# Performance work log

Measured on AMD Instinct MI355X. Metric: run time of the kernel, lower is better.

Reference implementation:

```python
import jax, jax.numpy as jnp
import numpy as np

NUM_Q = 8
K = 1024          # codebook_size
D = 256           # latent_dim
N = 65536         # number of vectors
COMMIT = 0.25


def setup_inputs() -> dict:
    key = jax.random.key(0)
    kz, kc = jax.random.split(key)
    z = jax.random.normal(kz, (N, D), dtype=jnp.float32)
    # torch init: uniform(-1/K, 1/K) per quantizer
    codebooks = jax.random.uniform(kc, (NUM_Q, K, D), dtype=jnp.float32,
                                   minval=-1.0 / K, maxval=1.0 / K)
    return {"z": z, "codebooks": codebooks}


def _vq_step(residual, W):
    # residual: [N, D], W: [K, D]
    # squared L2 distances [N, K] (same expansion as the torch code)
    d = (jnp.sum(residual ** 2, axis=1, keepdims=True)
         + jnp.sum(W ** 2, axis=1)
         - 2.0 * residual @ W.T)
    idx = jnp.argmin(d, axis=1)                      # [N]
    zq = W[idx]                                      # gather == one-hot @ W
    zq_ste = residual + jax.lax.stop_gradient(zq - residual)
    commitment = jnp.mean((jax.lax.stop_gradient(residual) - zq) ** 2)
    codebook_l = jnp.mean((residual - jax.lax.stop_gradient(zq)) ** 2)
    loss = codebook_l + COMMIT * commitment
    return zq_ste, idx, loss


def reference(z, codebooks):
    def step(residual, W):
        zq_ste, idx, loss = _vq_step(residual, W)
        residual_new = residual - jax.lax.stop_gradient(zq_ste)
        return residual_new, (zq_ste, idx, loss)

    _, (all_q, all_idx, losses) = jax.lax.scan(step, z, codebooks)
    z_reconstructed = jnp.sum(all_q, axis=0)          # [N, D]
    final_indices = all_idx.T[:, :, None]             # [N, Q, 1] (torch stacks [N,1] on dim=1)
    total_loss = jnp.sum(losses)
    return z_reconstructed, final_indices, total_loss
```

## Files before the change

### kernel.cpp

```cpp
#include <hip/hip_runtime.h>
#include <stdint.h>


#define NQ      8
#define KCODES  1024
#define DIM     256
#define NVEC    65536
#define ROWS    32
#define RST     260
#define CCH     32
#define CAP     32

typedef unsigned int u32;
typedef unsigned long long u64;
typedef unsigned short u16;
typedef short bf16x8 __attribute__((ext_vector_type(8)));
typedef float f32x4  __attribute__((ext_vector_type(4)));

__device__ float  g_norms[NQ * KCODES];
__device__ u32    g_nkmax;
__device__ double g_loss;
__device__ __align__(16) u16 g_wb[(size_t)NQ * KCODES * DIM];

__device__ __forceinline__ u16 bf16rne(float x){
    u32 u = __float_as_uint(x);
    return (u16)((u + 0x7FFFu + ((u >> 16) & 1u)) >> 16);
}

__device__ __forceinline__ void gload_lds16(const void* g, void* l){
    __builtin_amdgcn_global_load_lds(
        (const __attribute__((address_space(1))) u32*)g,
        (__attribute__((address_space(3))) u32*)l, 16, 0, 0);
}

__device__ __forceinline__ float np_sumsq128(const float* __restrict__ a){
    float r0,r1,r2,r3,r4,r5,r6,r7;
    {
        float4 v0 = *(const float4*)(a);
        float4 v1 = *(const float4*)(a + 4);
        r0 = __fmul_rn(v0.x,v0.x); r1 = __fmul_rn(v0.y,v0.y);
        r2 = __fmul_rn(v0.z,v0.z); r3 = __fmul_rn(v0.w,v0.w);
        r4 = __fmul_rn(v1.x,v1.x); r5 = __fmul_rn(v1.y,v1.y);
        r6 = __fmul_rn(v1.z,v1.z); r7 = __fmul_rn(v1.w,v1.w);
    }
    for (int i = 8; i < 128; i += 8){
        float4 v0 = *(const float4*)(a + i);
        float4 v1 = *(const float4*)(a + i + 4);
        r0 = __fadd_rn(r0, __fmul_rn(v0.x,v0.x));
        r1 = __fadd_rn(r1, __fmul_rn(v0.y,v0.y));
        r2 = __fadd_rn(r2, __fmul_rn(v0.z,v0.z));
        r3 = __fadd_rn(r3, __fmul_rn(v0.w,v0.w));
        r4 = __fadd_rn(r4, __fmul_rn(v1.x,v1.x));
        r5 = __fadd_rn(r5, __fmul_rn(v1.y,v1.y));
        r6 = __fadd_rn(r6, __fmul_rn(v1.z,v1.z));
        r7 = __fadd_rn(r7, __fmul_rn(v1.w,v1.w));
    }
    return __fadd_rn(__fadd_rn(__fadd_rn(r0,r1), __fadd_rn(r2,r3)),
                     __fadd_rn(__fadd_rn(r4,r5), __fadd_rn(r6,r7)));
}

__global__ void vq_zero(){ g_loss = 0.0; g_nkmax = 0u; }

__global__ void vq_norms_np(const float* __restrict__ cb){
    int row = blockIdx.x * 256 + threadIdx.x;
    const float* a = cb + (size_t)row * DIM;
    float n = __fadd_rn(np_sumsq128(a), np_sumsq128(a + 128));
    g_norms[row] = n;
    atomicMax(&g_nkmax, __float_as_uint(n));
}

__global__ void vq_prep_wb(const float* __restrict__ cb){
    int t = blockIdx.x * 256 + threadIdx.x;
    int code = t >> 5, s = t & 31;
    const float* src = cb + (size_t)code * DIM + s * 8;
    float4 v0 = *(const float4*)(src);
    float4 v1 = *(const float4*)(src + 4);
    u64 P0 =  (u64)bf16rne(v0.x)        | ((u64)bf16rne(v0.y) << 16)
           | ((u64)bf16rne(v0.z) << 32) | ((u64)bf16rne(v0.w) << 48);
    u64 P1 =  (u64)bf16rne(v1.x)        | ((u64)bf16rne(v1.y) << 16)
           | ((u64)bf16rne(v1.z) << 32) | ((u64)bf16rne(v1.w) << 48);
    u64* dst = (u64*)(g_wb + (size_t)code * DIM + ((s ^ (code & 7)) << 3));
    dst[0] = P0; dst[1] = P1;
}

__device__ __forceinline__ void ldsAtomicMinU64(u64* p, u64 v){
    u64 old = *p;
    while (v < old){
        u64 a = old;
        old = atomicCAS(p, a, v);
        if (old == a) break;
    }
}

__global__ __launch_bounds__(128)
void vq_main(const float* __restrict__ z, const float* __restrict__ cb,
             float* __restrict__ out)
{
    __shared__ __align__(16) float R[ROWS * RST];
    __shared__ __align__(16) u16   Wst[CCH * DIM];
    __shared__ float t1[ROWS];
    __shared__ u32   rminU[ROWS];
    __shared__ u32   cnt[ROWS];
    __shared__ u16   cand[ROWS * CAP];
    __shared__ u64   bestKey[ROWS];
    __shared__ int   bestk[ROWS];
    __shared__ int   idxs[ROWS * NQ];
    __shared__ int   off[ROWS + 1];
    __shared__ int   totalS, ovf;

    const int tid     = threadIdx.x;
    const int rowbase = blockIdx.x * ROWS;
    const int ct      = tid >> 6;
    const int lane    = tid & 63;
    const int l15     = lane & 15, lg = lane >> 4;
    const int urow    = tid >> 2, us = tid & 3;
    double lossAcc = 0.0;

#pragma unroll
    for (int l = 0; l < 16; ++l){
        int i = l * 128 + tid;
        int row = i >> 6, c4 = i & 63;
        float4 v = *(const float4*)(z + (size_t)(rowbase + row) * DIM + c4 * 4);
        *(float4*)(R + row * RST + c4 * 4) = v;
    }
    __syncthreads();

    const float sqnkmax = sqrtf(__uint_as_float(g_nkmax));

    for (int q = 0; q < NQ; ++q){
        if (tid < 64){
            float s = np_sumsq128(R + (tid >> 1) * RST + (tid & 1) * 128);
            float o = __shfl_xor(s, 1);
            if ((tid & 1) == 0) t1[tid >> 1] = __fadd_rn(s, o);
        }
        if (tid < ROWS){
            rminU[tid]   = 0x7f800000u;
            cnt[tid]     = 0u;
            bestKey[tid] = ~0ull;
        }
        __syncthreads();
        if (tid == 0 && q > 0)
            for (int r = 0; r < ROWS; ++r) lossAcc += (double)t1[r];

        bf16x8 a[2][8];
#pragma unroll
        for (int rt = 0; rt < 2; ++rt){
            const float* rr = R + (rt * 16 + l15) * RST + lg * 8;
#pragma unroll
            for (int ks = 0; ks < 8; ++ks){
                float4 v0 = *(const float4*)(rr + ks * 32);
                float4 v1 = *(const float4*)(rr + ks * 32 + 4);
                union { bf16x8 v; u64 p[2]; } u;
                u.p[0] =  (u64)bf16rne(v0.x)        | ((u64)bf16rne(v0.y) << 16)
                       | ((u64)bf16rne(v0.z) << 32) | ((u64)bf16rne(v0.w) << 48);
                u.p[1] =  (u64)bf16rne(v1.x)        | ((u64)bf16rne(v1.y) << 16)
                       | ((u64)bf16rne(v1.z) << 32) | ((u64)bf16rne(v1.w) << 48);
                a[rt][ks] = u.v;
            }
        }
        float t1r[2][4], delta[2][4];
#pragma unroll
        for (int rt = 0; rt < 2; ++rt)
#pragma unroll
            for (int j = 0; j < 4; ++j){
                t1r[rt][j]   = t1[rt * 16 + lg * 4 + j];
                delta[rt][j] = 0.02f * sqrtf(t1r[rt][j]) * sqnkmax + 3e-4f;
            }

        const char* wbq = (const char*)g_wb + (size_t)q * KCODES * DIM * 2;
        const int key = l15 & 7;

        for (int tt = 0; tt < 36; ++tt){
            int  cc      = (tt < 32) ? tt : (tt - 32);
            bool collect = (tt >= 4);
            {
                const char* src = wbq + (size_t)cc * (CCH * DIM * 2);
                char* dstb = (char*)Wst;
#pragma unroll
                for (int r = 0; r < 8; ++r){
                    int o = (r * 128 + tid) * 16;
                    gload_lds16(src + o, dstb + o);
                }
            }
            __syncthreads();

            int   codeL = ct * 16 + l15;
            float nk    = g_norms[q * KCODES + cc * CCH + codeL];
            const u16* wrow = Wst + codeL * DIM;
            f32x4 accA0 = {0,0,0,0}, accB0 = {0,0,0,0};
            f32x4 accA1 = {0,0,0,0}, accB1 = {0,0,0,0};
#pragma unroll
            for (int ks = 0; ks < 4; ++ks){
                bf16x8 blo = *(const bf16x8*)(wrow + (((ks * 4 + lg) ^ key) << 3));
                bf16x8 bhi = *(const bf16x8*)(wrow + ((((ks + 4) * 4 + lg) ^ key) << 3));
                accA0 = __builtin_amdgcn_mfma_f32_16x16x32_bf16(a[0][ks],     blo, accA0, 0, 0, 0);
                accB0 = __builtin_amdgcn_mfma_f32_16x16x32_bf16(a[0][ks + 4], bhi, accB0, 0, 0, 0);
                accA1 = __builtin_amdgcn_mfma_f32_16x16x32_bf16(a[1][ks],     blo, accA1, 0, 0, 0);
                accB1 = __builtin_amdgcn_mfma_f32_16x16x32_bf16(a[1][ks + 4], bhi, accB1, 0, 0, 0);
            }
            int codeg = cc * CCH + codeL;
#pragma unroll
            for (int rt = 0; rt < 2; ++rt){
                f32x4 sA = rt ? accA1 : accA0, sB = rt ? accB1 : accB0;
#pragma unroll
                for (int j = 0; j < 4; ++j){
                    float dest = (t1r[rt][j] + nk) - 2.0f * (sA[j] + sB[j]);
                    int   row  = rt * 16 + lg * 4 + j;
                    u32   curb = rminU[row];
                    float curf = __uint_as_float(curb);
                    if (dest < curf) atomicMin(&rminU[row], __float_as_uint(dest));
                    if (collect && dest <= curf + delta[rt][j]){
                        u32 slot = atomicAdd(&cnt[row], 1u);
                        if (slot < CAP) cand[row * CAP + slot] = (u16)codeg;
                    }
                }
            }
            __syncthreads();
        }

        if (tid == 0){
            int tot = 0, ov = 0;
            for (int r = 0; r < ROWS; ++r){
                off[r] = tot;
                int c = (int)cnt[r];
                if (c > CAP){ c = CAP; ov = 1; }
                tot += c;
            }
            off[ROWS] = tot; totalS = tot; ovf = ov;
        }
        __syncthreads();

        int nT = totalS;
        for (int t = tid; t < nT; t += 128){
            int r = 0;
            while (off[r + 1] <= t) ++r;
            int k = (int)cand[r * CAP + (t - off[r])];
            const float* wr = cb + ((size_t)q * KCODES + k) * DIM;
            const float* rr = R + r * RST;
            float dot = 0.f;
#pragma unroll 4
            for (int i = 0; i < 64; ++i){
                float4 rv = *(const float4*)(rr + i * 4);
                float4 wv = *(const float4*)(wr + i * 4);
                dot = __builtin_fmaf(rv.x, wv.x, dot);
                dot = __builtin_fmaf(rv.y, wv.y, dot);
                dot = __builtin_fmaf(rv.z, wv.z, dot);
                dot = __builtin_fmaf(rv.w, wv.w, dot);
            }
            float d = __fsub_rn(__fadd_rn(t1[r], g_norms[q * KCODES + k]),
                                __fmul_rn(2.0f, dot));
            ldsAtomicMinU64(&bestKey[r], ((u64)__float_as_uint(d) << 32) | (u32)k);
        }
        if (ovf){
            for (int r = 0; r < ROWS; ++r){
                if (cnt[r] > CAP){
                    for (int k = tid; k < KCODES; k += 128){
                        const float* wr = cb + ((size_t)q * KCODES + k) * DIM;
                        const float* rr = R + r * RST;
                        float dot = 0.f;
                        for (int i = 0; i < 64; ++i){
                            float4 rv = *(const float4*)(rr + i * 4);
                            float4 wv = *(const float4*)(wr + i * 4);
                            dot = __builtin_fmaf(rv.x, wv.x, dot);
                            dot = __builtin_fmaf(rv.y, wv.y, dot);
                            dot = __builtin_fmaf(rv.z, wv.z, dot);
                            dot = __builtin_fmaf(rv.w, wv.w, dot);
                        }
                        float d = __fsub_rn(__fadd_rn(t1[r], g_norms[q * KCODES + k]),
                                            __fmul_rn(2.0f, dot));
                        ldsAtomicMinU64(&bestKey[r], ((u64)__float_as_uint(d) << 32) | (u32)k);
                    }
                }
            }
        }
        __syncthreads();
        if (tid < ROWS){
            int k = (int)(bestKey[tid] & 0xFFFFFFFFull);
            bestk[tid] = k;
            idxs[tid * NQ + q] = k;
        }
        __syncthreads();

        {
            int k = bestk[urow];
            const float* wrow = cb + ((size_t)q * KCODES + k) * DIM;
#pragma unroll
            for (int j = 0; j < 16; ++j){
                int d0 = us * 4 + j * 16;
                float4 r4 = *(float4*)(R + urow * RST + d0);
                float4 wv = *(const float4*)(wrow + d0);
                float4 rn;
                rn.x = __fsub_rn(r4.x, __fadd_rn(r4.x, __fsub_rn(wv.x, r4.x)));
                rn.y = __fsub_rn(r4.y, __fadd_rn(r4.y, __fsub_rn(wv.y, r4.y)));
                rn.z = __fsub_rn(r4.z, __fadd_rn(r4.z, __fsub_rn(wv.z, r4.z)));
                rn.w = __fsub_rn(r4.w, __fadd_rn(r4.w, __fsub_rn(wv.w, r4.w)));
                *(float4*)(R + urow * RST + d0) = rn;
            }
        }
        __syncthreads();
    }

    if (tid < 64){
        float s = np_sumsq128(R + (tid >> 1) * RST + (tid & 1) * 128);
        float o = __shfl_xor(s, 1);
        if ((tid & 1) == 0) t1[tid >> 1] = __fadd_rn(s, o);
    }
    __syncthreads();
    if (tid == 0){
        for (int r = 0; r < ROWS; ++r) lossAcc += (double)t1[r];
        atomicAdd(&g_loss, lossAcc);
    }

    for (int e = tid; e < ROWS * NQ; e += 128){
        int row = e >> 3, qq = e & 7;
        out[(size_t)NVEC * DIM + ((size_t)rowbase + row) * NQ + qq] =
            (float)idxs[row * NQ + qq];
    }
    {
        size_t n = (size_t)rowbase + urow;
#pragma unroll
        for (int j = 0; j < 16; ++j){
            int d0 = us * 4 + j * 16;
            float4 zv = *(const float4*)(z + n * DIM + d0);
            float4 rv = *(const float4*)(R + urow * RST + d0);
            float4 ov;
            ov.x = __fsub_rn(zv.x, rv.x);
            ov.y = __fsub_rn(zv.y, rv.y);
            ov.z = __fsub_rn(zv.z, rv.z);
            ov.w = __fsub_rn(zv.w, rv.w);
            *(float4*)(out + n * DIM + d0) = ov;
        }
    }
}

__global__ void vq_loss_final(float* __restrict__ out){
    if (threadIdx.x == 0 && blockIdx.x == 0){
        double m = 1.25 * g_loss / ((double)NVEC * (double)DIM);
        out[(size_t)NVEC * DIM + (size_t)NVEC * NQ] = (float)m;
    }
}

extern "C" void kernel_launch(void* const* d_in, const int* in_sizes, int n_in,
                              void* d_out, int out_size, void* d_ws, size_t ws_size,
                              hipStream_t stream) {
    (void)in_sizes; (void)n_in; (void)out_size; (void)d_ws; (void)ws_size;
    const float* z  = (const float*)d_in[0];
    const float* cb = (const float*)d_in[1];
    float* out = (float*)d_out;

    hipLaunchKernelGGL(vq_zero,       dim3(1),    dim3(1),   0, stream);
    hipLaunchKernelGGL(vq_norms_np,   dim3(32),   dim3(256), 0, stream, cb);
    hipLaunchKernelGGL(vq_prep_wb,    dim3(1024), dim3(256), 0, stream, cb);
    hipLaunchKernelGGL(vq_main,       dim3(NVEC / ROWS), dim3(128), 0, stream, z, cb, out);
    hipLaunchKernelGGL(vq_loss_final, dim3(1),    dim3(64),  0, stream, out);
}
```

Measured before the change: 1.505 ms.

## Double the codebook chunk, register-prefetch next chunk, use 256 threads per block

Each block now runs 256 threads and handles 64 codes per chunk, with 4 waves each taking 16 codes. The direct global-to-LDS loads are replaced by a register prefetch: the next chunk is loaded into registers while the current chunk is computed, and the warm-up rescan shrinks to 2 chunks. The serial per-row candidate offset loop becomes a wave shuffle prefix scan, and the residual update and output loops use an XOR-permuted column mapping across 8 threads per row. The aim is to hide load latency and cut serial and barrier overhead, at the cost of more registers, a larger LDS tile and a risk of lower occupancy.

Result: slower. 2.836 ms (+88.4%).

```diff
diff --git a/kernel.cpp b/kernel.cpp
--- a/kernel.cpp
+++ b/kernel.cpp
@@ -8,7 +8,9 @@
 #define NVEC    65536
 #define ROWS    32
 #define RST     260
-#define CCH     32
+#define CCH     64
+#define NCH     (KCODES / CCH)
+#define WARM    2
 #define CAP     32
 
 typedef unsigned int u32;
@@ -25,12 +27,6 @@
 __device__ __forceinline__ u16 bf16rne(float x){
     u32 u = __float_as_uint(x);
     return (u16)((u + 0x7FFFu + ((u >> 16) & 1u)) >> 16);
-}
-
-__device__ __forceinline__ void gload_lds16(const void* g, void* l){
-    __builtin_amdgcn_global_load_lds(
-        (const __attribute__((address_space(1))) u32*)g,
-        (__attribute__((address_space(3))) u32*)l, 16, 0, 0);
 }
 
 __device__ __forceinline__ float np_sumsq128(const float* __restrict__ a){
@@ -92,7 +88,7 @@
     }
 }
 
-__global__ __launch_bounds__(128)
+__global__ __launch_bounds__(256, 2)
 void vq_main(const float* __restrict__ z, const float* __restrict__ cb,
              float* __restrict__ out)
 {
@@ -110,15 +106,17 @@
 
     const int tid     = threadIdx.x;
     const int rowbase = blockIdx.x * ROWS;
-    const int ct      = tid >> 6;
+    const int w       = tid >> 6;
     const int lane    = tid & 63;
     const int l15     = lane & 15, lg = lane >> 4;
-    const int urow    = tid >> 2, us = tid & 3;
+    const int key     = l15 & 7;
+    const int urow    = tid >> 3, us = tid & 7;
+    const int uperm   = (us ^ (urow & 7)) << 2;
     double lossAcc = 0.0;
 
 #pragma unroll
-    for (int l = 0; l < 16; ++l){
-        int i = l * 128 + tid;
+    for (int l = 0; l < 8; ++l){
+        int i = l * 256 + tid;
         int row = i >> 6, c4 = i & 63;
         float4 v = *(const float4*)(z + (size_t)(rowbase + row) * DIM + c4 * 4);
         *(float4*)(R + row * RST + c4 * 4) = v;
@@ -168,23 +166,31 @@
             }
 
         const char* wbq = (const char*)g_wb + (size_t)q * KCODES * DIM * 2;
-        const int key = l15 & 7;
-
-        for (int tt = 0; tt < 36; ++tt){
-            int  cc      = (tt < 32) ? tt : (tt - 32);
-            bool collect = (tt >= 4);
-            {
-                const char* src = wbq + (size_t)cc * (CCH * DIM * 2);
-                char* dstb = (char*)Wst;
-#pragma unroll
-                for (int r = 0; r < 8; ++r){
-                    int o = (r * 128 + tid) * 16;
-                    gload_lds16(src + o, dstb + o);
-                }
-            }
+
+        float4 pf[8];
+#pragma unroll
+        for (int r = 0; r < 8; ++r)
+            pf[r] = *(const float4*)(wbq + (size_t)(r * 256 + tid) * 16);
+
+        for (int tt = 0; tt < NCH + WARM; ++tt){
+            int  cc      = (tt < NCH) ? tt : (tt - NCH);
+            bool collect = (tt >= WARM);
+
             __syncthreads();
-
-            int   codeL = ct * 16 + l15;
+#pragma unroll
+            for (int r = 0; r < 8; ++r)
+                *(float4*)((char*)Wst + (size_t)(r * 256 + tid) * 16) = pf[r];
+            __syncthreads();
+
+            if (tt < NCH + WARM - 1){
+                int nc = (tt + 1 < NCH) ? tt + 1 : (tt + 1 - NCH);
+                const char* src = wbq + (size_t)nc * (CCH * DIM * 2);
+#pragma unroll
+                for (int r = 0; r < 8; ++r)
+                    pf[r] = *(const float4*)(src + (size_t)(r * 256 + tid) * 16);
+            }
+
+            int   codeL = w * 16 + l15;
             float nk    = g_norms[q * KCODES + cc * CCH + codeL];
             const u16* wrow = Wst + codeL * DIM;
             f32x4 accA0 = {0,0,0,0}, accB0 = {0,0,0,0};
@@ -215,23 +221,28 @@
                     }
                 }
             }
-            __syncthreads();
-        }
-
-        if (tid == 0){
-            int tot = 0, ov = 0;
-            for (int r = 0; r < ROWS; ++r){
-                off[r] = tot;
-                int c = (int)cnt[r];
-                if (c > CAP){ c = CAP; ov = 1; }
-                tot += c;
-            }
-            off[ROWS] = tot; totalS = tot; ovf = ov;
+        }
+        __syncthreads();
+
+        if (tid < 64){
+            int c    = (tid < 32) ? min((int)cnt[tid], CAP) : 0;
+            int over = (tid < 32) ? (cnt[tid] > CAP) : 0;
+            int x = c;
+#pragma unroll
+            for (int o = 1; o < 32; o <<= 1){
+                int y = __shfl_up(x, o);
+                if (tid >= o) x += y;
+            }
+            if (tid < 32) off[tid] = x - c;
+            if (tid == 31){ off[32] = x; totalS = x; }
+#pragma unroll
+            for (int o = 1; o < 32; o <<= 1) over |= __shfl_xor(over, o);
+            if (tid == 0) ovf = over;
         }
         __syncthreads();
 
         int nT = totalS;
-        for (int t = tid; t < nT; t += 128){
+        for (int t = tid; t < nT; t += 256){
             int r = 0;
             while (off[r + 1] <= t) ++r;
             int k = (int)cand[r * CAP + (t - off[r])];
@@ -254,7 +265,7 @@
         if (ovf){
             for (int r = 0; r < ROWS; ++r){
                 if (cnt[r] > CAP){
-                    for (int k = tid; k < KCODES; k += 128){
+                    for (int k = tid; k < KCODES; k += 256){
                         const float* wr = cb + ((size_t)q * KCODES + k) * DIM;
                         const float* rr = R + r * RST;
                         float dot = 0.f;
@@ -282,11 +293,11 @@
         __syncthreads();
 
         {
-            int k = bestk[urow];
-            const float* wrow = cb + ((size_t)q * KCODES + k) * DIM;
-#pragma unroll
-            for (int j = 0; j < 16; ++j){
-                int d0 = us * 4 + j * 16;
+            int kk = bestk[urow];
+            const float* wrow = cb + ((size_t)q * KCODES + kk) * DIM;
+#pragma unroll
+            for (int j = 0; j < 8; ++j){
+                int d0 = uperm + j * 32;
                 float4 r4 = *(float4*)(R + urow * RST + d0);
                 float4 wv = *(const float4*)(wrow + d0);
                 float4 rn;
@@ -311,16 +322,16 @@
         atomicAdd(&g_loss, lossAcc);
     }
 
-    for (int e = tid; e < ROWS * NQ; e += 128){
-        int row = e >> 3, qq = e & 7;
+    {
+        int row = tid >> 3, qq = tid & 7;
         out[(size_t)NVEC * DIM + ((size_t)rowbase + row) * NQ + qq] =
             (float)idxs[row * NQ + qq];
     }
     {
         size_t n = (size_t)rowbase + urow;
 #pragma unroll
-        for (int j = 0; j < 16; ++j){
-            int d0 = us * 4 + j * 16;
+        for (int j = 0; j < 8; ++j){
+            int d0 = uperm + j * 32;
             float4 zv = *(const float4*)(z + n * DIM + d0);
             float4 rv = *(const float4*)(R + urow * RST + d0);
             float4 ov;
@@ -351,6 +362,6 @@
     hipLaunchKernelGGL(vq_zero,       dim3(1),    dim3(1),   0, stream);
     hipLaunchKernelGGL(vq_norms_np,   dim3(32),   dim3(256), 0, stream, cb);
     hipLaunchKernelGGL(vq_prep_wb,    dim3(1024), dim3(256), 0, stream, cb);
-    hipLaunchKernelGGL(vq_main,       dim3(NVEC / ROWS), dim3(128), 0, stream, z, cb, out);
+    hipLaunchKernelGGL(vq_main,       dim3(NVEC / ROWS), dim3(256), 0, stream, z, cb, out);
     hipLaunchKernelGGL(vq_loss_final, dim3(1),    dim3(64),  0, stream, out);
 }
```

## Double-buffer codebook tiles in LDS and parallelize candidate offset scan

Applied to the files above, without the earlier changes.

Codebook chunks are now loaded into two alternating LDS buffers, so the next chunk's global-to-LDS copy is issued before the MFMA distance work on the current chunk. This removes one barrier per chunk and hides load latency behind compute. The serial single-thread prefix sum over per-row candidate counts is replaced by a wavefront shuffle scan, with an OR-reduction for the overflow flag. In exchange, the extra 16KB of LDS per block may lower the number of blocks resident per CU.

Result: slower. 1.870 ms (+24.2%).

```diff
diff --git a/kernel.cpp b/kernel.cpp
--- a/kernel.cpp
+++ b/kernel.cpp
@@ -9,6 +9,8 @@
 #define ROWS    32
 #define RST     260
 #define CCH     32
+#define NCH     (KCODES / CCH)
+#define WARM    4
 #define CAP     32
 
 typedef unsigned int u32;
@@ -97,7 +99,7 @@
              float* __restrict__ out)
 {
     __shared__ __align__(16) float R[ROWS * RST];
-    __shared__ __align__(16) u16   Wst[CCH * DIM];
+    __shared__ __align__(16) u16   Wst[2][CCH * DIM];
     __shared__ float t1[ROWS];
     __shared__ u32   rminU[ROWS];
     __shared__ u32   cnt[ROWS];
@@ -113,6 +115,7 @@
     const int ct      = tid >> 6;
     const int lane    = tid & 63;
     const int l15     = lane & 15, lg = lane >> 4;
+    const int key     = l15 & 7;
     const int urow    = tid >> 2, us = tid & 3;
     double lossAcc = 0.0;
 
@@ -168,25 +171,36 @@
             }
 
         const char* wbq = (const char*)g_wb + (size_t)q * KCODES * DIM * 2;
-        const int key = l15 & 7;
-
-        for (int tt = 0; tt < 36; ++tt){
-            int  cc      = (tt < 32) ? tt : (tt - 32);
-            bool collect = (tt >= 4);
-            {
-                const char* src = wbq + (size_t)cc * (CCH * DIM * 2);
-                char* dstb = (char*)Wst;
+
+        {
+            char* dstb = (char*)Wst[0];
+#pragma unroll
+            for (int r = 0; r < 8; ++r){
+                int o = (r * 128 + tid) * 16;
+                gload_lds16(wbq + o, dstb + o);
+            }
+        }
+        __syncthreads();
+
+        for (int tt = 0; tt < NCH + WARM; ++tt){
+            int  cc      = (tt < NCH) ? tt : (tt - NCH);
+            int  cur     = tt & 1;
+            bool collect = (tt >= WARM);
+
+            if (tt + 1 < NCH + WARM){
+                int nc = (tt + 1 < NCH) ? tt + 1 : (tt + 1 - NCH);
+                const char* src = wbq + (size_t)nc * (CCH * DIM * 2);
+                char* dstb = (char*)Wst[cur ^ 1];
 #pragma unroll
                 for (int r = 0; r < 8; ++r){
                     int o = (r * 128 + tid) * 16;
                     gload_lds16(src + o, dstb + o);
                 }
             }
-            __syncthreads();
 
             int   codeL = ct * 16 + l15;
             float nk    = g_norms[q * KCODES + cc * CCH + codeL];
-            const u16* wrow = Wst + codeL * DIM;
+            const u16* wrow = Wst[cur] + codeL * DIM;
             f32x4 accA0 = {0,0,0,0}, accB0 = {0,0,0,0};
             f32x4 accA1 = {0,0,0,0}, accB1 = {0,0,0,0};
 #pragma unroll
@@ -218,15 +232,20 @@
             __syncthreads();
         }
 
-        if (tid == 0){
-            int tot = 0, ov = 0;
-            for (int r = 0; r < ROWS; ++r){
-                off[r] = tot;
-                int c = (int)cnt[r];
-                if (c > CAP){ c = CAP; ov = 1; }
-                tot += c;
-            }
-            off[ROWS] = tot; totalS = tot; ovf = ov;
+        if (tid < 64){
+            int c    = (tid < 32) ? min((int)cnt[tid], CAP) : 0;
+            int over = (tid < 32) ? (cnt[tid] > CAP) : 0;
+            int x = c;
+#pragma unroll
+            for (int o = 1; o < 32; o <<= 1){
+                int y = __shfl_up(x, o);
+                if (tid >= o) x += y;
+            }
+            if (tid < 32) off[tid] = x - c;
+            if (tid == 31){ off[32] = x; totalS = x; }
+#pragma unroll
+            for (int o = 1; o < 32; o <<= 1) over |= __shfl_xor(over, o);
+            if (tid == 0) ovf = over;
         }
         __syncthreads();
 
```
